# Performance work log

Measured on AMD Instinct MI355X. Metric: run time of the kernel, lower is better.

The kernel has to match this reference:

```python
import jax, jax.numpy as jnp
import numpy as np
from jax import lax

STRIDES = (8, 16, 32)
NUM_CLASSES = 80
TOPK = 1000
CONF_THRESH = 0.05
NMS_THRESH = 0.6


def setup_inputs() -> dict:
    key = jax.random.key(0)
    ks = jax.random.split(key, 10)
    hw = [(256, 256), (128, 128), (64, 64)]
    inp = {}
    for lv, (h, w) in enumerate(hw):
        inp[f"cls_pred_{lv}"] = jax.random.normal(ks[3 * lv + 0], (NUM_CLASSES, h, w), jnp.float32)
        inp[f"reg_pred_{lv}"] = jax.random.normal(ks[3 * lv + 1], (4, h, w), jnp.float32)
        inp[f"ctn_pred_{lv}"] = jax.random.normal(ks[3 * lv + 2], (1, h, w), jnp.float32)
    inp["scales"] = jax.random.uniform(ks[9], (3,), jnp.float32)
    return inp


def _level_decode(cls_p, reg_p, ctn_p, scale, stride):
    # cls_p: [C,H,W] -> flatten to [M,C] matching torch permute(1,2,0).view(-1,C)
    C, H, W = cls_p.shape
    cls = jnp.transpose(cls_p, (1, 2, 0)).reshape(-1, C)          # [M,C]
    reg = jnp.transpose(reg_p, (1, 2, 0)).reshape(-1, 4)          # [M,4]
    reg = jax.nn.relu(reg * scale) * stride                       # Scale + relu + stride
    ctn = jnp.transpose(ctn_p, (1, 2, 0)).reshape(-1, 1)          # [M,1]
    joint = jnp.sqrt(jax.nn.sigmooid(cls) * jax.nn.sigmoid(ctn)) if False else \
        jnp.sqrt(jax.nn.sigmoid(cls) * jax.nn.sigmoid(ctn))      # [M,C]
    scores = jnp.max(joint, axis=-1)                              # [M]
    labels = jnp.argmax(joint, axis=-1)                           # [M]
    ay, ax = jnp.meshgrid(jnp.arange(H), jnp.arange(W), indexing='ij')
    anchors = (jnp.stack([ax, ay], -1).reshape(-1, 2).astype(cls.dtype) + 0.5) * stride  # [M,2]
    # per-level topk (M > TOPK for all levels here)
    scores, idx = lax.top_k(scores, TOPK)
    labels = labels[idx]
    reg = reg[idx]
    anchors = anchors[idx]
    boxes = jnp.concatenate([anchors - reg[:, :2], anchors + reg[:, 2:]], axis=-1)  # x1y1x2y2
    return scores, labels, boxes


def _nms(boxes, scores):
    # Faithful port of the pure-python NMS: fixed-shape keep mask, sorted order.
    N = boxes.shape[0]
    order = jnp.argsort(-scores)
    b = boxes[order]
    x1, y1, x2, y2 = b[:, 0], b[:, 1], b[:, 2], b[:, 3]
    areas = (x2 - x1) * (y2 - y1)
    xx1 = jnp.maximum(x1[:, None], x1[None, :])
    yy1 = jnp.maximum(y1[:, None], y1[None, :])
    xx2 = jnp.minimum(x2[:, None], x2[None, :])
    yy2 = jnp.minimum(y2[:, None], y2[None, :])
    w = jnp.maximum(1e-10, xx2 - xx1)
    h = jnp.maximum(1e-10, yy2 - yy1)
    inter = w * h
    iou = inter / (areas[:, None] + areas[None, :] - inter + 1e-14)  # [N,N]
    idxs = jnp.arange(N)

    def body(i, keep):
        sup = (iou[i] > NMS_THRESH) & (idxs > i) & keep[i]
        return keep & ~sup

    keep = lax.fori_loop(0, N, body, jnp.ones((N,), bool))
    return order, keep


def reference(cls_pred_0, cls_pred_1, cls_pred_2,
              reg_pred_0, reg_pred_1, reg_pred_2,
              ctn_pred_0, ctn_pred_1, ctn_pred_2, scales):
    cls_l = [cls_pred_0, cls_pred_1, cls_pred_2]
    reg_l = [reg_pred_0, reg_pred_1, reg_pred_2]
    ctn_l = [ctn_pred_0, ctn_pred_1, ctn_pred_2]
    all_s, all_l, all_b = [], [], []
    for lv in range(3):
        s, lb, bx = _level_decode(cls_l[lv], reg_l[lv], ctn_l[lv], scales[lv], float(STRIDES[lv]))
        all_s.append(s); all_l.append(lb); all_b.append(bx)
    scores = jnp.concatenate(all_s)   # [3000]
    labels = jnp.concatenate(all_l)
    boxes = jnp.concatenate(all_b)    # [3000,4]
    order, keep = _nms(boxes, scores)
    scores_s = scores[order]
    labels_s = labels[order]
    boxes_s = boxes[order]
    keep = keep & (scores_s > CONF_THRESH)
    return boxes_s, scores_s, labels_s, keep
```

## Files before the change

kernel.cpp:

```cpp
#include <hip/hip_runtime.h>
#include <cmath>
#include <stdint.h>

#define NPTS   86016
#define NB     (1 << 18)
#define NCB    1024
#define K_TOP  1000
#define NOUT   3000
#define NWORDS 47
#define NTILE  47
#define CAND_CAP 16384
#define ECAP   8192
#define FCAP   1024
#define SPPB   64

#define HIST_OFF   0
#define CH_OFF     (NB * 3 * 4)
#define CNT_OFF    (CH_OFF + NCB * 3 * 4)
#define MEMSET_BYTES (CNT_OFF + 64)
#define KEYS_OFF   (CNT_OFF + 64)
#define LAB_OFF    (KEYS_OFF + NPTS * 8)
#define SURE_OFF   (LAB_OFF + NPTS * 4)
#define CAND_OFF   (SURE_OFF + 3 * 1024 * 8)
#define SURV_OFF   (CAND_OFF + 3 * CAND_CAP * 8)
#define EDGE_OFF   (SURV_OFF + NOUT * 8 + 64)
#define FLAG_OFF   (EDGE_OFF + ECAP * 4)

__device__ __forceinline__ float sig_f32_stepwise(float x) {
    float e = (float)exp(-(double)x);
    return 1.0f / (1.0f + e);
}

__device__ __forceinline__ void locate(int g, int& lv, int& p, int& HW) {
    if (g < 65536)      { lv = 0; p = g;         HW = 65536; }
    else if (g < 81920) { lv = 1; p = g - 65536; HW = 16384; }
    else                { lv = 2; p = g - 81920; HW = 4096;  }
}

__global__ __launch_bounds__(256) void score_kernel(
        const float* __restrict__ cls0, const float* __restrict__ cls1,
        const float* __restrict__ cls2,
        const float* __restrict__ ctn0, const float* __restrict__ ctn1,
        const float* __restrict__ ctn2,
        unsigned long long* __restrict__ keys, int* __restrict__ labels,
        int* __restrict__ hist, int* __restrict__ chist,
        int* __restrict__ cnt, unsigned* __restrict__ flags) {
    __shared__ float pm[5 * SPPB], pv[5 * SPPB];
    __shared__ int pidx[5 * SPPB];
    __shared__ int lch[NCB];
    const int tid = threadIdx.x;
    const int base = blockIdx.x * SPPB;
    for (int i = tid; i < NCB; i += 256) lch[i] = 0;
    for (int it = tid; it < 5 * SPPB; it += 256) {
        int c = it / SPPB, pt = it - c * SPPB;
        int g = base + pt, lv, p, HW;
        locate(g, lv, p, HW);
        const float* cls = (lv == 0) ? cls0 : ((lv == 1) ? cls1 : cls2);
        const float* bp = cls + (size_t)c * 16 * HW + p;
        float x[16];
#pragma unroll
        for (int cc = 0; cc < 16; cc++) x[cc] = bp[(size_t)cc * HW];
        float m = -INFINITY, v = -INFINITY; int idx = 0;
#pragma unroll
        for (int cc = 0; cc < 16; cc++)
            if (x[cc] > m) { v = m; m = x[cc]; idx = c * 16 + cc; }
        pm[it] = m; pv[it] = v; pidx[it] = idx;
    }
    __syncthreads();
    if (tid < SPPB) {
        int g = base + tid, lv, p, HW;
        locate(g, lv, p, HW);
        const float* ctn = (lv == 0) ? ctn0 : ((lv == 1) ? ctn1 : ctn2);
        float m = -INFINITY, v = -INFINITY; int idx = 0;
#pragma unroll
        for (int k = 0; k < 5; k++) {
            float bm = pm[k * SPPB + tid];
            float bv = pv[k * SPPB + tid];
            int bidx = pidx[k * SPPB + tid];
            if (bm > m) { v = fmaxf(m, bv); m = bm; idx = bidx; }
        }
        float sc = sig_f32_stepwise(ctn[p]);
        float sM = sig_f32_stepwise(m);
        float jm = __fsqrt_rn(sM * sc);
        float sV = sig_f32_stepwise(v);
        float jv = __fsqrt_rn(sV * sc);
        if (jv == jm) {
            int f = atomicAdd(&cnt[13], 1);
            if (f < FCAP) flags[f] = (unsigned)g;
        }
        unsigned int bits = __float_as_uint(jm);
        keys[g] = ((unsigned long long)bits << 32) | (0xFFFFFFFFu - (unsigned)g);
        labels[g] = idx;
        atomicAdd(&hist[lv * NB + (int)(bits >> 12)], 1);
        atomicAdd(&lch[(int)(bits >> 20)], 1);
    }
    __syncthreads();
    int lv0, p0, HW0; locate(base, lv0, p0, HW0);
    for (int i = tid; i < NCB; i += 256) {
        int v = lch[i];
        if (v) atomicAdd(&chist[lv0 * NCB + i], v);
    }
}

__global__ __launch_bounds__(1024) void thresh_kernel(
        const float* __restrict__ cls0, const float* __restrict__ cls1,
        const float* __restrict__ cls2,
        const float* __restrict__ ctn0, const float* __restrict__ ctn1,
        const float* __restrict__ ctn2,
        const int* __restrict__ hist, const int* __restrict__ chist,
        int* __restrict__ cnt,
        const unsigned* __restrict__ flags, int* __restrict__ labels) {
    int bid = blockIdx.x, tid = threadIdx.x;
    if (bid < 3) {
        int lv = bid;
        const int* h = hist + lv * NB;
        __shared__ int part[1024];
        __shared__ int s_chunk, s_above;
        __shared__ int bins[257];
        part[tid] = chist[lv * NCB + tid];
        __syncthreads();
        for (int off = 1; off < 1024; off <<= 1) {
            int v = part[tid] + ((tid + off < 1024) ? part[tid + off] : 0);
            __syncthreads(); part[tid] = v; __syncthreads();
        }
        int nxt = (tid < 1023) ? part[tid + 1] : 0;
        if (part[tid] >= K_TOP && nxt < K_TOP) { s_chunk = tid; s_above = nxt; }
        __syncthreads();
        int chunk = s_chunk, above = s_above;
        if (tid < 256) bins[tid] = h[chunk * 256 + tid];
        __syncthreads();
        for (int off = 1; off < 256; off <<= 1) {
            int v = 0;
            if (tid < 256) v = bins[tid] + ((tid + off < 256) ? bins[tid + off] : 0);
            __syncthreads(); if (tid < 256) bins[tid] = v; __syncthreads();
        }
        if (tid < 256) {
            int ge    = above + bins[tid];
            int genxt = above + ((tid < 255) ? bins[tid + 1] : 0);
            if (ge >= K_TOP && genxt < K_TOP) {
                cnt[6 + lv] = chunk * 256 + tid;
                cnt[9 + lv] = K_TOP - genxt;
            }
        }
    } else {
        int nf = cnt[13]; if (nf > FCAP) nf = FCAP;
        int wave = tid >> 6, lane = tid & 63;
        for (int f = wave; f < nf; f += 16) {
            int g = (int)flags[f], lv, p, HW;
            locate(g, lv, p, HW);
            const float* cls = (lv == 0) ? cls0 : ((lv == 1) ? cls1 : cls2);
            const float* ctn = (lv == 0) ? ctn0 : ((lv == 1) ? ctn1 : ctn2);
            float sc = sig_f32_stepwise(ctn[p]);
            float bestv = -1.0f; int besti = 127;
            {
                float s = sig_f32_stepwise(cls[(size_t)lane * HW + p]);
                float sj = __fsqrt_rn(s * sc);
                bestv = sj; besti = lane;
            }
            if (lane < 16) {
                int c2 = lane + 64;
                float s = sig_f32_stepwise(cls[(size_t)c2 * HW + p]);
                float sj = __fsqrt_rn(s * sc);
                if (sj > bestv) { bestv = sj; besti = c2; }
            }
            for (int off = 32; off; off >>= 1) {
                float ov = __shfl_xor(bestv, off, 64);
                int   oi = __shfl_xor(besti, off, 64);
                if (ov > bestv || (ov == bestv && oi < besti)) { bestv = ov; besti = oi; }
            }
            if (lane == 0) labels[g] = besti;
        }
    }
}

__global__ void compact_kernel(const unsigned long long* __restrict__ keys,
                               int* __restrict__ cnt,
                               unsigned long long* __restrict__ sure,
                               unsigned long long* __restrict__ cand) {
    int g = blockIdx.x * blockDim.x + threadIdx.x;
    if (g >= NPTS) return;
    int lv = (g < 65536) ? 0 : (g < 81920 ? 1 : 2);
    unsigned long long key = keys[g];
    int bin = (int)(key >> 44);
    int B = cnt[6 + lv];
    if (bin > B) {
        int i = atomicAdd(&cnt[0 + lv], 1);
        sure[lv * 1024 + i] = key;
    } else if (bin == B) {
        int i = atomicAdd(&cnt[3 + lv], 1);
        if (i < CAND_CAP) cand[lv * CAND_CAP + i] = key;
    }
}

__global__ void select_kernel(const int* __restrict__ cnt,
                              const unsigned long long* __restrict__ sure,
                              unsigned long long* __restrict__ cand,
                              unsigned long long* __restrict__ surv) {
    int lv = blockIdx.x, tid = threadIdx.x;
    unsigned long long* c = cand + lv * CAND_CAP;
    int n = cnt[3 + lv]; if (n > CAND_CAP) n = CAND_CAP;
    int R = cnt[9 + lv];
    int Ca = K_TOP - R;
    int m = 1; while (m < n) m <<= 1;
    for (int t = n + tid; t < m; t += 1024) c[t] = 0ULL;
    __syncthreads();
    for (int k = 2; k <= m; k <<= 1)
        for (int j = k >> 1; j > 0; j >>= 1) {
            for (int t = tid; t < m; t += 1024) {
                int l = t ^ j;
                if (l > t) {
                    unsigned long long a = c[t], b = c[l];
                    if (((t & k) == 0) ? (a < b) : (a > b)) { c[t] = b; c[l] = a; }
                }
            }
            __syncthreads();
        }
    __shared__ unsigned long long s[1024];
    s[tid] = (tid < Ca) ? sure[lv * 1024 + tid]
                        : ((tid < K_TOP) ? c[tid - Ca] : 0ULL);
    __syncthreads();
    for (int k = 2; k <= 1024; k <<= 1)
        for (int j = k >> 1; j > 0; j >>= 1) {
            int l = tid ^ j;
            if (l > tid) {
                unsigned long long a = s[tid], b = s[l];
                if (((tid & k) == 0) ? (a < b) : (a > b)) { s[tid] = b; s[l] = a; }
            }
            __syncthreads();
        }
    if (tid < K_TOP) surv[lv * K_TOP + tid] = s[tid];
}

__global__ __launch_bounds__(1024) void merge_emit_kernel(
        const unsigned long long* __restrict__ surv,
        const int* __restrict__ labels,
        const float* __restrict__ reg0, const float* __restrict__ reg1,
        const float* __restrict__ reg2,
        const float* __restrict__ scales,
        float* __restrict__ out) {
    __shared__ unsigned long long L[3][1024];
    __shared__ unsigned long long s[NOUT];
    int tid = threadIdx.x;
#pragma unroll
    for (int lv = 0; lv < 3; lv++)
        L[lv][tid] = (tid < K_TOP) ? surv[lv * K_TOP + tid] : 0ULL;
    __syncthreads();
    for (int e = tid; e < NOUT; e += 1024) {
        int a = e / K_TOP, i = e - a * K_TOP;
        unsigned long long key = L[a][i];
        int rank = i;
#pragma unroll
        for (int b = 0; b < 3; b++) {
            if (b == a) continue;
            int lo = 0, hi = K_TOP;
            while (lo < hi) {
                int mid = (lo + hi) >> 1;
                if (L[b][mid] > key) lo = mid + 1; else hi = mid;
            }
            rank += lo;
        }
        s[rank] = key;
    }
    __syncthreads();
    for (int r = tid; r < NOUT; r += 1024) {
        unsigned long long key = s[r];
        unsigned int bits = (unsigned)(key >> 32);
        float score = __uint_as_float(bits);
        unsigned int g = 0xFFFFFFFFu - (unsigned)(key & 0xFFFFFFFFULL);
        int lv, p;
        if (g < 65536u)      { lv = 0; p = (int)g; }
        else if (g < 81920u) { lv = 1; p = (int)g - 65536; }
        else                 { lv = 2; p = (int)g - 81920; }
        const float* rp = (lv == 0) ? reg0 : ((lv == 1) ? reg1 : reg2);
        int HW = (lv == 0) ? 65536 : ((lv == 1) ? 16384 : 4096);
        int W = 256 >> lv;
        float strideF = (float)(8 << lv);
        float scale = scales[lv];
        int x = p & (W - 1);
        int y = p >> (8 - lv);
        float r0 = fmaxf(0.0f, rp[0 * HW + p] * scale) * strideF;
        float r1 = fmaxf(0.0f, rp[1 * HW + p] * scale) * strideF;
        float r2 = fmaxf(0.0f, rp[2 * HW + p] * scale) * strideF;
        float r3 = fmaxf(0.0f, rp[3 * HW + p] * scale) * strideF;
        float ax = ((float)x + 0.5f) * strideF;
        float ay = ((float)y + 0.5f) * strideF;
        out[r * 4 + 0] = ax - r0;
        out[r * 4 + 1] = ay - r1;
        out[r * 4 + 2] = ax + r2;
        out[r * 4 + 3] = ay + r3;
        out[12000 + r] = score;
        out[15000 + r] = (float)labels[g];
    }
}

__global__ __launch_bounds__(256) void edge_kernel(const float* __restrict__ out,
                                                   unsigned* __restrict__ edges_g,
                                                   int* __restrict__ cnt) {
    __shared__ float x1[128], y1[128], x2[128], y2[128];
    int t = blockIdx.x, tid = threadIdx.x;
    int ta = 0, rem = t;
    while (rem >= NTILE - ta) { rem -= NTILE - ta; ta++; }
    int tb = ta + rem;
    if (tid < 64) {
        int gi = ta * 64 + tid;
        if (gi < NOUT) {
            float4 b = ((const float4*)out)[gi];
            x1[tid] = b.x; y1[tid] = b.y; x2[tid] = b.z; y2[tid] = b.w;
        }
    } else if (tid < 128) {
        int gj = tb * 64 + (tid - 64);
        if (gj < NOUT) {
            float4 b = ((const float4*)out)[gj];
            x1[tid] = b.x; y1[tid] = b.y; x2[tid] = b.z; y2[tid] = b.w;
        }
    }
    __syncthreads();
#pragma unroll
    for (int q = 0; q < 16; q++) {
        int idx = q * 256 + tid;
        int ii = idx >> 6, jj = idx & 63;
        int i = ta * 64 + ii, j = tb * 64 + jj;
        if (i < j && j < NOUT) {
            float ai = (x2[ii] - x1[ii]) * (y2[ii] - y1[ii]);
            float aj = (x2[64 + jj] - x1[64 + jj]) * (y2[64 + jj] - y1[64 + jj]);
            float xx1 = fmaxf(x1[ii], x1[64 + jj]), yy1 = fmaxf(y1[ii], y1[64 + jj]);
            float xx2 = fminf(x2[ii], x2[64 + jj]), yy2 = fminf(y2[ii], y2[64 + jj]);
            float ww = fmaxf(1e-10f, xx2 - xx1);
            float hh = fmaxf(1e-10f, yy2 - yy1);
            float inter = ww * hh;
            float iou = inter / (((ai + aj) - inter) + 1e-14f);
            if ((double)iou > 0.6) {
                int e = atomicAdd(&cnt[12], 1);
                if (e < ECAP) edges_g[e] = ((unsigned)i << 12) | (unsigned)j;
            }
        }
    }
}

__global__ __launch_bounds__(1024) void nms_sparse_kernel(
        const unsigned* __restrict__ edges_g,
        const int* __restrict__ cnt,
        const float* __restrict__ scores_s,
        float* __restrict__ keep_out) {
    __shared__ unsigned ed[ECAP];
    __shared__ unsigned long long supLds[NWORDS];
    int tid = threadIdx.x;
    int E = cnt[12]; if (E > ECAP) E = ECAP;
    int m = 1; while (m < E) m <<= 1;
    for (int t = tid; t < m; t += 1024) ed[t] = (t < E) ? edges_g[t] : 0xFFFFFFFFu;
    __syncthreads();
    for (int k = 2; k <= m; k <<= 1)
        for (int j = k >> 1; j > 0; j >>= 1) {
            for (int t = tid; t < m; t += 1024) {
                int l = t ^ j;
                if (l > t) {
                    unsigned a = ed[t], b = ed[l];
                    if (((t & k) == 0) ? (a > b) : (a < b)) { ed[t] = b; ed[l] = a; }
                }
            }
            __syncthreads();
        }
    if (tid < 64) {
        int lane = tid;
        unsigned long long supW = 0ULL;
        int ep = 0;
        for (int c = 0; c < NWORDS; c++) {
            unsigned long long cw = __shfl(supW, c, 64);
            int hi = (c + 1) * 64;
            while (ep < E) {
                unsigned k = ed[ep];
                int i = (int)(k >> 12);
                if (i >= hi) break;
                int j = (int)(k & 4095);
                if (!((cw >> (i & 63)) & 1ULL)) {
                    if ((j >> 6) == c) cw |= 1ULL << (j & 63);
                    else if (lane == (j >> 6)) supW |= 1ULL << (j & 63);
                }
                ep++;
            }
            if (lane == c) supW = cw;
        }
        if (lane < NWORDS) supLds[lane] = supW;
    }
    __syncthreads();
    for (int j = tid; j < NOUT; j += 1024) {
        bool s = (supLds[j >> 6] >> (j & 63)) & 1ULL;
        float scv = scores_s[j];
        keep_out[j] = (!s && ((double)scv > 0.05)) ? 1.0f : 0.0f;
    }
}

extern "C" void kernel_launch(void* const* d_in, const int* in_sizes, int n_in,
                              void* d_out, int out_size, void* d_ws, size_t ws_size,
                              hipStream_t stream) {
    const float* cls0 = (const float*)d_in[0];
    const float* reg0 = (const float*)d_in[1];
    const float* ctn0 = (const float*)d_in[2];
    const float* cls1 = (const float*)d_in[3];
    const float* reg1 = (const float*)d_in[4];
    const float* ctn1 = (const float*)d_in[5];
    const float* cls2 = (const float*)d_in[6];
    const float* reg2 = (const float*)d_in[7];
    const float* ctn2 = (const float*)d_in[8];
    const float* scales = (const float*)d_in[9];

    char* ws = (char*)d_ws;
    int* hist = (int*)(ws + HIST_OFF);
    int* chist = (int*)(ws + CH_OFF);
    int* cnt  = (int*)(ws + CNT_OFF);
    unsigned long long* keys = (unsigned long long*)(ws + KEYS_OFF);
    int* labels = (int*)(ws + LAB_OFF);
    unsigned long long* sure = (unsigned long long*)(ws + SURE_OFF);
    unsigned long long* cand = (unsigned long long*)(ws + CAND_OFF);
    unsigned long long* surv = (unsigned long long*)(ws + SURV_OFF);
    unsigned* edges = (unsigned*)(ws + EDGE_OFF);
    unsigned* flags = (unsigned*)(ws + FLAG_OFF);
    float* out = (float*)d_out;

    hipMemsetAsync(ws, 0, MEMSET_BYTES, stream);

    score_kernel<<<NPTS / SPPB, 256, 0, stream>>>(cls0, cls1, cls2, ctn0, ctn1, ctn2,
                                                  keys, labels, hist, chist, cnt, flags);
    thresh_kernel<<<4, 1024, 0, stream>>>(cls0, cls1, cls2, ctn0, ctn1, ctn2,
                                          hist, chist, cnt, flags, labels);
    compact_kernel<<<(NPTS + 255) / 256, 256, 0, stream>>>(keys, cnt, sure, cand);
    select_kernel<<<3, 1024, 0, stream>>>(cnt, sure, cand, surv);
    merge_emit_kernel<<<1, 1024, 0, stream>>>(surv, labels, reg0, reg1, reg2, scales, out);
    edge_kernel<<<NTILE * (NTILE + 1) / 2, 256, 0, stream>>>(out, edges, cnt);
    nms_sparse_kernel<<<1, 1024, 0, stream>>>(edges, cnt, out + 12000, out + 18000);
}
```

Baseline: 194.6 us.

## Fuse all pipeline stages into one persistent kernel with grid barriers

Merges the seven separate kernels into a single persistent kernel of 256 blocks of 1024 threads, with stages separated by a software grid barrier built on atomics in workspace memory. The scoring stage now splits each point's 80 classes across two lanes and combines them with a shuffle. The per-block shared-memory coarse histogram is replaced by direct global atomics, and edge tiles are processed by 8 teams per block. This is meant to remove the launch gaps between the many small serial stages. In exchange it relies on all 256 blocks being co-resident, and most blocks sit idle at several barriers while single-block stages run.

```diff
diff --git a/kernel.cpp b/kernel.cpp
--- a/kernel.cpp
+++ b/kernel.cpp
@@ -9,16 +9,19 @@
 #define NOUT   3000
 #define NWORDS 47
 #define NTILE  47
+#define NTILES (NTILE * (NTILE + 1) / 2)
 #define CAND_CAP 16384
 #define ECAP   8192
 #define FCAP   1024
-#define SPPB   64
+#define GRID   256
+#define BLOCK  1024
 
 #define HIST_OFF   0
 #define CH_OFF     (NB * 3 * 4)
 #define CNT_OFF    (CH_OFF + NCB * 3 * 4)
-#define MEMSET_BYTES (CNT_OFF + 64)
-#define KEYS_OFF   (CNT_OFF + 64)
+#define BAR_OFF    (CNT_OFF + 64)
+#define MEMSET_BYTES (BAR_OFF + 128)
+#define KEYS_OFF   (BAR_OFF + 128)
 #define LAB_OFF    (KEYS_OFF + NPTS * 8)
 #define SURE_OFF   (LAB_OFF + NPTS * 4)
 #define CAND_OFF   (SURE_OFF + 3 * 1024 * 8)
@@ -37,112 +40,131 @@
     else                { lv = 2; p = g - 81920; HW = 4096;  }
 }
 
-__global__ __launch_bounds__(256) void score_kernel(
+__device__ __forceinline__ void gsync(int* bar, int nblk) {
+    __syncthreads();
+    if (threadIdx.x == 0) {
+        __threadfence();
+        int* cntp = bar;
+        int* genp = bar + 16;
+        int g = __hip_atomic_load(genp, __ATOMIC_RELAXED, __HIP_MEMORY_SCOPE_AGENT);
+        int prev = __hip_atomic_fetch_add(cntp, 1, __ATOMIC_RELAXED, __HIP_MEMORY_SCOPE_AGENT);
+        if (prev == nblk - 1) {
+            __hip_atomic_store(cntp, 0, __ATOMIC_RELAXED, __HIP_MEMORY_SCOPE_AGENT);
+            __threadfence();
+            __hip_atomic_store(genp, g + 1, __ATOMIC_RELAXED, __HIP_MEMORY_SCOPE_AGENT);
+        } else {
+            while (__hip_atomic_load(genp, __ATOMIC_RELAXED, __HIP_MEMORY_SCOPE_AGENT) == g)
+                __builtin_amdgcn_s_sleep(2);
+        }
+        __threadfence();
+    }
+    __syncthreads();
+}
+
+__global__ __launch_bounds__(1024, 4) void fcos_mega(
         const float* __restrict__ cls0, const float* __restrict__ cls1,
         const float* __restrict__ cls2,
         const float* __restrict__ ctn0, const float* __restrict__ ctn1,
         const float* __restrict__ ctn2,
-        unsigned long long* __restrict__ keys, int* __restrict__ labels,
-        int* __restrict__ hist, int* __restrict__ chist,
-        int* __restrict__ cnt, unsigned* __restrict__ flags) {
-    __shared__ float pm[5 * SPPB], pv[5 * SPPB];
-    __shared__ int pidx[5 * SPPB];
-    __shared__ int lch[NCB];
+        const float* __restrict__ reg0, const float* __restrict__ reg1,
+        const float* __restrict__ reg2,
+        const float* __restrict__ scales, char* ws, float* out) {
     const int tid = threadIdx.x;
-    const int base = blockIdx.x * SPPB;
-    for (int i = tid; i < NCB; i += 256) lch[i] = 0;
-    for (int it = tid; it < 5 * SPPB; it += 256) {
-        int c = it / SPPB, pt = it - c * SPPB;
-        int g = base + pt, lv, p, HW;
-        locate(g, lv, p, HW);
-        const float* cls = (lv == 0) ? cls0 : ((lv == 1) ? cls1 : cls2);
-        const float* bp = cls + (size_t)c * 16 * HW + p;
-        float x[16];
-#pragma unroll
-        for (int cc = 0; cc < 16; cc++) x[cc] = bp[(size_t)cc * HW];
-        float m = -INFINITY, v = -INFINITY; int idx = 0;
-#pragma unroll
-        for (int cc = 0; cc < 16; cc++)
-            if (x[cc] > m) { v = m; m = x[cc]; idx = c * 16 + cc; }
-        pm[it] = m; pv[it] = v; pidx[it] = idx;
-    }
-    __syncthreads();
-    if (tid < SPPB) {
-        int g = base + tid, lv, p, HW;
-        locate(g, lv, p, HW);
-        const float* ctn = (lv == 0) ? ctn0 : ((lv == 1) ? ctn1 : ctn2);
-        float m = -INFINITY, v = -INFINITY; int idx = 0;
-#pragma unroll
-        for (int k = 0; k < 5; k++) {
-            float bm = pm[k * SPPB + tid];
-            float bv = pv[k * SPPB + tid];
-            int bidx = pidx[k * SPPB + tid];
-            if (bm > m) { v = fmaxf(m, bv); m = bm; idx = bidx; }
-        }
-        float sc = sig_f32_stepwise(ctn[p]);
-        float sM = sig_f32_stepwise(m);
-        float jm = __fsqrt_rn(sM * sc);
-        float sV = sig_f32_stepwise(v);
-        float jv = __fsqrt_rn(sV * sc);
-        if (jv == jm) {
-            int f = atomicAdd(&cnt[13], 1);
-            if (f < FCAP) flags[f] = (unsigned)g;
-        }
-        unsigned int bits = __float_as_uint(jm);
-        keys[g] = ((unsigned long long)bits << 32) | (0xFFFFFFFFu - (unsigned)g);
-        labels[g] = idx;
-        atomicAdd(&hist[lv * NB + (int)(bits >> 12)], 1);
-        atomicAdd(&lch[(int)(bits >> 20)], 1);
-    }
-    __syncthreads();
-    int lv0, p0, HW0; locate(base, lv0, p0, HW0);
-    for (int i = tid; i < NCB; i += 256) {
-        int v = lch[i];
-        if (v) atomicAdd(&chist[lv0 * NCB + i], v);
-    }
-}
-
-__global__ __launch_bounds__(1024) void thresh_kernel(
-        const float* __restrict__ cls0, const float* __restrict__ cls1,
-        const float* __restrict__ cls2,
-        const float* __restrict__ ctn0, const float* __restrict__ ctn1,
-        const float* __restrict__ ctn2,
-        const int* __restrict__ hist, const int* __restrict__ chist,
-        int* __restrict__ cnt,
-        const unsigned* __restrict__ flags, int* __restrict__ labels) {
-    int bid = blockIdx.x, tid = threadIdx.x;
+    const int bid = blockIdx.x;
+    const int nblk = gridDim.x;
+
+    int* hist = (int*)(ws + HIST_OFF);
+    int* chist = (int*)(ws + CH_OFF);
+    int* cnt = (int*)(ws + CNT_OFF);
+    int* bar = (int*)(ws + BAR_OFF);
+    unsigned long long* keys = (unsigned long long*)(ws + KEYS_OFF);
+    int* labels = (int*)(ws + LAB_OFF);
+    unsigned long long* sure = (unsigned long long*)(ws + SURE_OFF);
+    unsigned long long* cand = (unsigned long long*)(ws + CAND_OFF);
+    unsigned long long* surv = (unsigned long long*)(ws + SURV_OFF);
+    unsigned* edges_g = (unsigned*)(ws + EDGE_OFF);
+    unsigned* flags = (unsigned*)(ws + FLAG_OFF);
+
+    __shared__ union {
+        struct { int part[1024]; int bins[257]; int s_chunk; int s_above; } th;
+        struct { unsigned long long s[1024]; } sel;
+        struct { unsigned long long L[3][1024]; unsigned long long s[NOUT]; } mg;
+        struct { float x1[8][128], y1[8][128], x2[8][128], y2[8][128]; } eg;
+        struct { unsigned ed[ECAP]; unsigned long long supLds[NWORDS]; } nm;
+    } sh;
+
+    {
+        const int u = bid * BLOCK + tid;
+        if (u < 2 * NPTS) {
+            const int g = u >> 1, half = u & 1;
+            int lv, p, HW; locate(g, lv, p, HW);
+            const float* cls = (lv == 0) ? cls0 : ((lv == 1) ? cls1 : cls2);
+            const float* bp = cls + (size_t)(half * 40) * HW + p;
+            float m = -INFINITY, v = -INFINITY; int idx = half * 40;
+#pragma unroll
+            for (int cb = 0; cb < 5; cb++) {
+                float x[8];
+#pragma unroll
+                for (int cc = 0; cc < 8; cc++) x[cc] = bp[(size_t)(cb * 8 + cc) * HW];
+#pragma unroll
+                for (int cc = 0; cc < 8; cc++)
+                    if (x[cc] > m) { v = m; m = x[cc]; idx = half * 40 + cb * 8 + cc; }
+            }
+            float om = __shfl_xor(m, 1, 64);
+            float ov = __shfl_xor(v, 1, 64);
+            int   oi = __shfl_xor(idx, 1, 64);
+            if (half == 0) {
+                if (om > m) { v = fmaxf(m, ov); m = om; idx = oi; }
+                else        { v = fmaxf(v, om); }
+                const float* ctn = (lv == 0) ? ctn0 : ((lv == 1) ? ctn1 : ctn2);
+                float sc = sig_f32_stepwise(ctn[p]);
+                float sM = sig_f32_stepwise(m);
+                float jm = __fsqrt_rn(sM * sc);
+                float sV = sig_f32_stepwise(v);
+                float jv = __fsqrt_rn(sV * sc);
+                if (jv == jm) {
+                    int f = atomicAdd(&cnt[13], 1);
+                    if (f < FCAP) flags[f] = (unsigned)g;
+                }
+                unsigned int bits = __float_as_uint(jm);
+                keys[g] = ((unsigned long long)bits << 32) | (0xFFFFFFFFu - (unsigned)g);
+                labels[g] = idx;
+                atomicAdd(&hist[lv * NB + (int)(bits >> 12)], 1);
+                atomicAdd(&chist[lv * NCB + (int)(bits >> 20)], 1);
+            }
+        }
+    }
+    gsync(bar, nblk);
+
     if (bid < 3) {
         int lv = bid;
         const int* h = hist + lv * NB;
-        __shared__ int part[1024];
-        __shared__ int s_chunk, s_above;
-        __shared__ int bins[257];
-        part[tid] = chist[lv * NCB + tid];
+        sh.th.part[tid] = chist[lv * NCB + tid];
         __syncthreads();
         for (int off = 1; off < 1024; off <<= 1) {
-            int v = part[tid] + ((tid + off < 1024) ? part[tid + off] : 0);
-            __syncthreads(); part[tid] = v; __syncthreads();
-        }
-        int nxt = (tid < 1023) ? part[tid + 1] : 0;
-        if (part[tid] >= K_TOP && nxt < K_TOP) { s_chunk = tid; s_above = nxt; }
-        __syncthreads();
-        int chunk = s_chunk, above = s_above;
-        if (tid < 256) bins[tid] = h[chunk * 256 + tid];
+            int v = sh.th.part[tid] + ((tid + off < 1024) ? sh.th.part[tid + off] : 0);
+            __syncthreads(); sh.th.part[tid] = v; __syncthreads();
+        }
+        int nxt = (tid < 1023) ? sh.th.part[tid + 1] : 0;
+        if (sh.th.part[tid] >= K_TOP && nxt < K_TOP) { sh.th.s_chunk = tid; sh.th.s_above = nxt; }
+        __syncthreads();
+        int chunk = sh.th.s_chunk, above = sh.th.s_above;
+        if (tid < 256) sh.th.bins[tid] = h[chunk * 256 + tid];
         __syncthreads();
         for (int off = 1; off < 256; off <<= 1) {
             int v = 0;
-            if (tid < 256) v = bins[tid] + ((tid + off < 256) ? bins[tid + off] : 0);
-            __syncthreads(); if (tid < 256) bins[tid] = v; __syncthreads();
+            if (tid < 256) v = sh.th.bins[tid] + ((tid + off < 256) ? sh.th.bins[tid + off] : 0);
+            __syncthreads(); if (tid < 256) sh.th.bins[tid] = v; __syncthreads();
         }
         if (tid < 256) {
-            int ge    = above + bins[tid];
-            int genxt = above + ((tid < 255) ? bins[tid + 1] : 0);
+            int ge    = above + sh.th.bins[tid];
+            int genxt = above + ((tid < 255) ? sh.th.bins[tid + 1] : 0);
             if (ge >= K_TOP && genxt < K_TOP) {
                 cnt[6 + lv] = chunk * 256 + tid;
                 cnt[9 + lv] = K_TOP - genxt;
             }
         }
-    } else {
+    } else if (bid == 3) {
         int nf = cnt[13]; if (nf > FCAP) nf = FCAP;
         int wave = tid >> 6, lane = tid & 63;
         for (int f = wave; f < nf; f += 16) {
@@ -171,222 +193,213 @@
             if (lane == 0) labels[g] = besti;
         }
     }
-}
-
-__global__ void compact_kernel(const unsigned long long* __restrict__ keys,
-                               int* __restrict__ cnt,
-                               unsigned long long* __restrict__ sure,
-                               unsigned long long* __restrict__ cand) {
-    int g = blockIdx.x * blockDim.x + threadIdx.x;
-    if (g >= NPTS) return;
-    int lv = (g < 65536) ? 0 : (g < 81920 ? 1 : 2);
-    unsigned long long key = keys[g];
-    int bin = (int)(key >> 44);
-    int B = cnt[6 + lv];
-    if (bin > B) {
-        int i = atomicAdd(&cnt[0 + lv], 1);
-        sure[lv * 1024 + i] = key;
-    } else if (bin == B) {
-        int i = atomicAdd(&cnt[3 + lv], 1);
-        if (i < CAND_CAP) cand[lv * CAND_CAP + i] = key;
-    }
-}
-
-__global__ void select_kernel(const int* __restrict__ cnt,
-                              const unsigned long long* __restrict__ sure,
-                              unsigned long long* __restrict__ cand,
-                              unsigned long long* __restrict__ surv) {
-    int lv = blockIdx.x, tid = threadIdx.x;
-    unsigned long long* c = cand + lv * CAND_CAP;
-    int n = cnt[3 + lv]; if (n > CAND_CAP) n = CAND_CAP;
-    int R = cnt[9 + lv];
-    int Ca = K_TOP - R;
-    int m = 1; while (m < n) m <<= 1;
-    for (int t = n + tid; t < m; t += 1024) c[t] = 0ULL;
-    __syncthreads();
-    for (int k = 2; k <= m; k <<= 1)
-        for (int j = k >> 1; j > 0; j >>= 1) {
-            for (int t = tid; t < m; t += 1024) {
-                int l = t ^ j;
-                if (l > t) {
-                    unsigned long long a = c[t], b = c[l];
-                    if (((t & k) == 0) ? (a < b) : (a > b)) { c[t] = b; c[l] = a; }
-                }
-            }
-            __syncthreads();
-        }
-    __shared__ unsigned long long s[1024];
-    s[tid] = (tid < Ca) ? sure[lv * 1024 + tid]
-                        : ((tid < K_TOP) ? c[tid - Ca] : 0ULL);
-    __syncthreads();
-    for (int k = 2; k <= 1024; k <<= 1)
-        for (int j = k >> 1; j > 0; j >>= 1) {
-            int l = tid ^ j;
-            if (l > tid) {
-                unsigned long long a = s[tid], b = s[l];
-                if (((tid & k) == 0) ? (a < b) : (a > b)) { s[tid] = b; s[l] = a; }
-            }
-            __syncthreads();
-        }
-    if (tid < K_TOP) surv[lv * K_TOP + tid] = s[tid];
-}
-
-__global__ __launch_bounds__(1024) void merge_emit_kernel(
-        const unsigned long long* __restrict__ surv,
-        const int* __restrict__ labels,
-        const float* __restrict__ reg0, const float* __restrict__ reg1,
-        const float* __restrict__ reg2,
-        const float* __restrict__ scales,
-        float* __restrict__ out) {
-    __shared__ unsigned long long L[3][1024];
-    __shared__ unsigned long long s[NOUT];
-    int tid = threadIdx.x;
-#pragma unroll
-    for (int lv = 0; lv < 3; lv++)
-        L[lv][tid] = (tid < K_TOP) ? surv[lv * K_TOP + tid] : 0ULL;
-    __syncthreads();
-    for (int e = tid; e < NOUT; e += 1024) {
-        int a = e / K_TOP, i = e - a * K_TOP;
-        unsigned long long key = L[a][i];
-        int rank = i;
-#pragma unroll
-        for (int b = 0; b < 3; b++) {
-            if (b == a) continue;
-            int lo = 0, hi = K_TOP;
-            while (lo < hi) {
-                int mid = (lo + hi) >> 1;
-                if (L[b][mid] > key) lo = mid + 1; else hi = mid;
-            }
-            rank += lo;
-        }
-        s[rank] = key;
-    }
-    __syncthreads();
-    for (int r = tid; r < NOUT; r += 1024) {
-        unsigned long long key = s[r];
-        unsigned int bits = (unsigned)(key >> 32);
-        float score = __uint_as_float(bits);
-        unsigned int g = 0xFFFFFFFFu - (unsigned)(key & 0xFFFFFFFFULL);
-        int lv, p;
-        if (g < 65536u)      { lv = 0; p = (int)g; }
-        else if (g < 81920u) { lv = 1; p = (int)g - 65536; }
-        else                 { lv = 2; p = (int)g - 81920; }
-        const float* rp = (lv == 0) ? reg0 : ((lv == 1) ? reg1 : reg2);
-        int HW = (lv == 0) ? 65536 : ((lv == 1) ? 16384 : 4096);
-        int W = 256 >> lv;
-        float strideF = (float)(8 << lv);
-        float scale = scales[lv];
-        int x = p & (W - 1);
-        int y = p >> (8 - lv);
-        float r0 = fmaxf(0.0f, rp[0 * HW + p] * scale) * strideF;
-        float r1 = fmaxf(0.0f, rp[1 * HW + p] * scale) * strideF;
-        float r2 = fmaxf(0.0f, rp[2 * HW + p] * scale) * strideF;
-        float r3 = fmaxf(0.0f, rp[3 * HW + p] * scale) * strideF;
-        float ax = ((float)x + 0.5f) * strideF;
-        float ay = ((float)y + 0.5f) * strideF;
-        out[r * 4 + 0] = ax - r0;
-        out[r * 4 + 1] = ay - r1;
-        out[r * 4 + 2] = ax + r2;
-        out[r * 4 + 3] = ay + r3;
-        out[12000 + r] = score;
-        out[15000 + r] = (float)labels[g];
-    }
-}
-
-__global__ __launch_bounds__(256) void edge_kernel(const float* __restrict__ out,
-                                                   unsigned* __restrict__ edges_g,
-                                                   int* __restrict__ cnt) {
-    __shared__ float x1[128], y1[128], x2[128], y2[128];
-    int t = blockIdx.x, tid = threadIdx.x;
-    int ta = 0, rem = t;
-    while (rem >= NTILE - ta) { rem -= NTILE - ta; ta++; }
-    int tb = ta + rem;
-    if (tid < 64) {
-        int gi = ta * 64 + tid;
-        if (gi < NOUT) {
-            float4 b = ((const float4*)out)[gi];
-            x1[tid] = b.x; y1[tid] = b.y; x2[tid] = b.z; y2[tid] = b.w;
-        }
-    } else if (tid < 128) {
-        int gj = tb * 64 + (tid - 64);
-        if (gj < NOUT) {
-            float4 b = ((const float4*)out)[gj];
-            x1[tid] = b.x; y1[tid] = b.y; x2[tid] = b.z; y2[tid] = b.w;
-        }
-    }
-    __syncthreads();
-#pragma unroll
-    for (int q = 0; q < 16; q++) {
-        int idx = q * 256 + tid;
-        int ii = idx >> 6, jj = idx & 63;
-        int i = ta * 64 + ii, j = tb * 64 + jj;
-        if (i < j && j < NOUT) {
-            float ai = (x2[ii] - x1[ii]) * (y2[ii] - y1[ii]);
-            float aj = (x2[64 + jj] - x1[64 + jj]) * (y2[64 + jj] - y1[64 + jj]);
-            float xx1 = fmaxf(x1[ii], x1[64 + jj]), yy1 = fmaxf(y1[ii], y1[64 + jj]);
-            float xx2 = fminf(x2[ii], x2[64 + jj]), yy2 = fminf(y2[ii], y2[64 + jj]);
-            float ww = fmaxf(1e-10f, xx2 - xx1);
-            float hh = fmaxf(1e-10f, yy2 - yy1);
-            float inter = ww * hh;
-            float iou = inter / (((ai + aj) - inter) + 1e-14f);
-            if ((double)iou > 0.6) {
-                int e = atomicAdd(&cnt[12], 1);
-                if (e < ECAP) edges_g[e] = ((unsigned)i << 12) | (unsigned)j;
-            }
-        }
-    }
-}
-
-__global__ __launch_bounds__(1024) void nms_sparse_kernel(
-        const unsigned* __restrict__ edges_g,
-        const int* __restrict__ cnt,
-        const float* __restrict__ scores_s,
-        float* __restrict__ keep_out) {
-    __shared__ unsigned ed[ECAP];
-    __shared__ unsigned long long supLds[NWORDS];
-    int tid = threadIdx.x;
-    int E = cnt[12]; if (E > ECAP) E = ECAP;
-    int m = 1; while (m < E) m <<= 1;
-    for (int t = tid; t < m; t += 1024) ed[t] = (t < E) ? edges_g[t] : 0xFFFFFFFFu;
-    __syncthreads();
-    for (int k = 2; k <= m; k <<= 1)
-        for (int j = k >> 1; j > 0; j >>= 1) {
-            for (int t = tid; t < m; t += 1024) {
-                int l = t ^ j;
-                if (l > t) {
-                    unsigned a = ed[t], b = ed[l];
-                    if (((t & k) == 0) ? (a > b) : (a < b)) { ed[t] = b; ed[l] = a; }
-                }
-            }
-            __syncthreads();
-        }
-    if (tid < 64) {
-        int lane = tid;
-        unsigned long long supW = 0ULL;
-        int ep = 0;
-        for (int c = 0; c < NWORDS; c++) {
-            unsigned long long cw = __shfl(supW, c, 64);
-            int hi = (c + 1) * 64;
-            while (ep < E) {
-                unsigned k = ed[ep];
-                int i = (int)(k >> 12);
-                if (i >= hi) break;
-                int j = (int)(k & 4095);
-                if (!((cw >> (i & 63)) & 1ULL)) {
-                    if ((j >> 6) == c) cw |= 1ULL << (j & 63);
-                    else if (lane == (j >> 6)) supW |= 1ULL << (j & 63);
-                }
-                ep++;
-            }
-            if (lane == c) supW = cw;
-        }
-        if (lane < NWORDS) supLds[lane] = supW;
-    }
-    __syncthreads();
-    for (int j = tid; j < NOUT; j += 1024) {
-        bool s = (supLds[j >> 6] >> (j & 63)) & 1ULL;
-        float scv = scores_s[j];
-        keep_out[j] = (!s && ((double)scv > 0.05)) ? 1.0f : 0.0f;
+    gsync(bar, nblk);
+
+    {
+        int g = bid * BLOCK + tid;
+        if (g < NPTS) {
+            int lv = (g < 65536) ? 0 : (g < 81920 ? 1 : 2);
+            unsigned long long key = keys[g];
+            int bin = (int)(key >> 44);
+            int B = cnt[6 + lv];
+            if (bin > B) {
+                int i = atomicAdd(&cnt[0 + lv], 1);
+                sure[lv * 1024 + i] = key;
+            } else if (bin == B) {
+                int i = atomicAdd(&cnt[3 + lv], 1);
+                if (i < CAND_CAP) cand[lv * CAND_CAP + i] = key;
+            }
+        }
+    }
+    gsync(bar, nblk);
+
+    if (bid < 3) {
+        int lv = bid;
+        unsigned long long* c = cand + lv * CAND_CAP;
+        int n = cnt[3 + lv]; if (n > CAND_CAP) n = CAND_CAP;
+        int R = cnt[9 + lv];
+        int Ca = K_TOP - R;
+        int m = 1; while (m < n) m <<= 1;
+        for (int t = n + tid; t < m; t += 1024) c[t] = 0ULL;
+        __syncthreads();
+        for (int k = 2; k <= m; k <<= 1)
+            for (int j = k >> 1; j > 0; j >>= 1) {
+                for (int t = tid; t < m; t += 1024) {
+                    int l = t ^ j;
+                    if (l > t) {
+                        unsigned long long a = c[t], b = c[l];
+                        if (((t & k) == 0) ? (a < b) : (a > b)) { c[t] = b; c[l] = a; }
+                    }
+                }
+                __syncthreads();
+            }
+        sh.sel.s[tid] = (tid < Ca) ? sure[lv * 1024 + tid]
+                                   : ((tid < K_TOP) ? c[tid - Ca] : 0ULL);
+        __syncthreads();
+        for (int k = 2; k <= 1024; k <<= 1)
+            for (int j = k >> 1; j > 0; j >>= 1) {
+                int l = tid ^ j;
+                if (l > tid) {
+                    unsigned long long a = sh.sel.s[tid], b = sh.sel.s[l];
+                    if (((tid & k) == 0) ? (a < b) : (a > b)) { sh.sel.s[tid] = b; sh.sel.s[l] = a; }
+                }
+                __syncthreads();
+            }
+        if (tid < K_TOP) surv[lv * K_TOP + tid] = sh.sel.s[tid];
+    }
+    gsync(bar, nblk);
+
+    if (bid == 0) {
+#pragma unroll
+        for (int lv = 0; lv < 3; lv++)
+            sh.mg.L[lv][tid] = (tid < K_TOP) ? surv[lv * K_TOP + tid] : 0ULL;
+        __syncthreads();
+        for (int e = tid; e < NOUT; e += 1024) {
+            int a = e / K_TOP, i = e - a * K_TOP;
+            unsigned long long key = sh.mg.L[a][i];
+            int rank = i;
+#pragma unroll
+            for (int b = 0; b < 3; b++) {
+                if (b == a) continue;
+                int lo = 0, hi = K_TOP;
+                while (lo < hi) {
+                    int mid = (lo + hi) >> 1;
+                    if (sh.mg.L[b][mid] > key) lo = mid + 1; else hi = mid;
+                }
+                rank += lo;
+            }
+            sh.mg.s[rank] = key;
+        }
+        __syncthreads();
+        for (int r = tid; r < NOUT; r += 1024) {
+            unsigned long long key = sh.mg.s[r];
+            unsigned int bits = (unsigned)(key >> 32);
+            float score = __uint_as_float(bits);
+            unsigned int g = 0xFFFFFFFFu - (unsigned)(key & 0xFFFFFFFFULL);
+            int lv, p;
+            if (g < 65536u)      { lv = 0; p = (int)g; }
+            else if (g < 81920u) { lv = 1; p = (int)g - 65536; }
+            else                 { lv = 2; p = (int)g - 81920; }
+            const float* rp = (lv == 0) ? reg0 : ((lv == 1) ? reg1 : reg2);
+            int HW = (lv == 0) ? 65536 : ((lv == 1) ? 16384 : 4096);
+            int W = 256 >> lv;
+            float strideF = (float)(8 << lv);
+            float scale = scales[lv];
+            int x = p & (W - 1);
+            int y = p >> (8 - lv);
+            float r0 = fmaxf(0.0f, rp[0 * HW + p] * scale) * strideF;
+            float r1 = fmaxf(0.0f, rp[1 * HW + p] * scale) * strideF;
+            float r2 = fmaxf(0.0f, rp[2 * HW + p] * scale) * strideF;
+            float r3 = fmaxf(0.0f, rp[3 * HW + p] * scale) * strideF;
+            float ax = ((float)x + 0.5f) * strideF;
+            float ay = ((float)y + 0.5f) * strideF;
+            out[r * 4 + 0] = ax - r0;
+            out[r * 4 + 1] = ay - r1;
+            out[r * 4 + 2] = ax + r2;
+            out[r * 4 + 3] = ay + r3;
+            out[12000 + r] = score;
+            out[15000 + r] = (float)labels[g];
+        }
+    }
+    gsync(bar, nblk);
+
+    {
+        int team = tid >> 7, lt = tid & 127;
+        int t = bid * 8 + team;
+        int ta = 0, tb = 0;
+        bool act = (t < NTILES);
+        if (act) {
+            int rem = t;
+            while (rem >= NTILE - ta) { rem -= NTILE - ta; ta++; }
+            tb = ta + rem;
+            if (lt < 64) {
+                int gi = ta * 64 + lt;
+                if (gi < NOUT) {
+                    float4 b = ((const float4*)out)[gi];
+                    sh.eg.x1[team][lt] = b.x; sh.eg.y1[team][lt] = b.y;
+                    sh.eg.x2[team][lt] = b.z; sh.eg.y2[team][lt] = b.w;
+                }
+            } else {
+                int gj = tb * 64 + (lt - 64);
+                if (gj < NOUT) {
+                    float4 b = ((const float4*)out)[gj];
+                    sh.eg.x1[team][lt] = b.x; sh.eg.y1[team][lt] = b.y;
+                    sh.eg.x2[team][lt] = b.z; sh.eg.y2[team][lt] = b.w;
+                }
+            }
+        }
+        __syncthreads();
+        if (act) {
+#pragma unroll
+            for (int q = 0; q < 32; q++) {
+                int idx = q * 128 + lt;
+                int ii = idx >> 6, jj = idx & 63;
+                int i = ta * 64 + ii, j = tb * 64 + jj;
+                if (i < j && j < NOUT) {
+                    float ai = (sh.eg.x2[team][ii] - sh.eg.x1[team][ii]) * (sh.eg.y2[team][ii] - sh.eg.y1[team][ii]);
+                    float aj = (sh.eg.x2[team][64 + jj] - sh.eg.x1[team][64 + jj]) * (sh.eg.y2[team][64 + jj] - sh.eg.y1[team][64 + jj]);
+                    float xx1 = fmaxf(sh.eg.x1[team][ii], sh.eg.x1[team][64 + jj]);
+                    float yy1 = fmaxf(sh.eg.y1[team][ii], sh.eg.y1[team][64 + jj]);
+                    float xx2 = fminf(sh.eg.x2[team][ii], sh.eg.x2[team][64 + jj]);
+                    float yy2 = fminf(sh.eg.y2[team][ii], sh.eg.y2[team][64 + jj]);
+                    float ww = fmaxf(1e-10f, xx2 - xx1);
+                    float hh = fmaxf(1e-10f, yy2 - yy1);
+                    float inter = ww * hh;
+                    float iou = inter / (((ai + aj) - inter) + 1e-14f);
+                    if ((double)iou > 0.6) {
+                        int e = atomicAdd(&cnt[12], 1);
+                        if (e < ECAP) edges_g[e] = ((unsigned)i << 12) | (unsigned)j;
+                    }
+                }
+            }
+        }
+    }
+    gsync(bar, nblk);
+
+    if (bid == 0) {
+        int E = cnt[12]; if (E > ECAP) E = ECAP;
+        int m = 1; while (m < E) m <<= 1;
+        for (int t = tid; t < m; t += 1024) sh.nm.ed[t] = (t < E) ? edges_g[t] : 0xFFFFFFFFu;
+        __syncthreads();
+        for (int k = 2; k <= m; k <<= 1)
+            for (int j = k >> 1; j > 0; j >>= 1) {
+                for (int t = tid; t < m; t += 1024) {
+                    int l = t ^ j;
+                    if (l > t) {
+                        unsigned a = sh.nm.ed[t], b = sh.nm.ed[l];
+                        if (((t & k) == 0) ? (a > b) : (a < b)) { sh.nm.ed[t] = b; sh.nm.ed[l] = a; }
+                    }
+                }
+                __syncthreads();
+            }
+        if (tid < 64) {
+            int lane = tid;
+            unsigned long long supW = 0ULL;
+            int ep = 0;
+            for (int c = 0; c < NWORDS; c++) {
+                unsigned long long cw = __shfl(supW, c, 64);
+                int hi = (c + 1) * 64;
+                while (ep < E) {
+                    unsigned kk = sh.nm.ed[ep];
+                    int i = (int)(kk >> 12);
+                    if (i >= hi) break;
+                    int j = (int)(kk & 4095);
+                    if (!((cw >> (i & 63)) & 1ULL)) {
+                        if ((j >> 6) == c) cw |= 1ULL << (j & 63);
+                        else if (lane == (j >> 6)) supW |= 1ULL << (j & 63);
+                    }
+                    ep++;
+                }
+                if (lane == c) supW = cw;
+            }
+            if (lane < NWORDS) sh.nm.supLds[lane] = supW;
+        }
+        __syncthreads();
+        for (int j = tid; j < NOUT; j += 1024) {
+            bool s = (sh.nm.supLds[j >> 6] >> (j & 63)) & 1ULL;
+            float scv = out[12000 + j];
+            out[18000 + j] = (!s && ((double)scv > 0.05)) ? 1.0f : 0.0f;
+        }
     }
 }
 
@@ -405,27 +418,10 @@
     const float* scales = (const float*)d_in[9];
 
     char* ws = (char*)d_ws;
-    int* hist = (int*)(ws + HIST_OFF);
-    int* chist = (int*)(ws + CH_OFF);
-    int* cnt  = (int*)(ws + CNT_OFF);
-    unsigned long long* keys = (unsigned long long*)(ws + KEYS_OFF);
-    int* labels = (int*)(ws + LAB_OFF);
-    unsigned long long* sure = (unsigned long long*)(ws + SURE_OFF);
-    unsigned long long* cand = (unsigned long long*)(ws + CAND_OFF);
-    unsigned long long* surv = (unsigned long long*)(ws + SURV_OFF);
-    unsigned* edges = (unsigned*)(ws + EDGE_OFF);
-    unsigned* flags = (unsigned*)(ws + FLAG_OFF);
     float* out = (float*)d_out;
 
     hipMemsetAsync(ws, 0, MEMSET_BYTES, stream);
 
-    score_kernel<<<NPTS / SPPB, 256, 0, stream>>>(cls0, cls1, cls2, ctn0, ctn1, ctn2,
-                                                  keys, labels, hist, chist, cnt, flags);
-    thresh_kernel<<<4, 1024, 0, stream>>>(cls0, cls1, cls2, ctn0, ctn1, ctn2,
-                                          hist, chist, cnt, flags, labels);
-    compact_kernel<<<(NPTS + 255) / 256, 256, 0, stream>>>(keys, cnt, sure, cand);
-    select_kernel<<<3, 1024, 0, stream>>>(cnt, sure, cand, surv);
-    merge_emit_kernel<<<1, 1024, 0, stream>>>(surv, labels, reg0, reg1, reg2, scales, out);
-    edge_kernel<<<NTILE * (NTILE + 1) / 2, 256, 0, stream>>>(out, edges, cnt);
-    nms_sparse_kernel<<<1, 1024, 0, stream>>>(edges, cnt, out + 12000, out + 18000);
+    fcos_mega<<<GRID, BLOCK, 0, stream>>>(cls0, cls1, cls2, ctn0, ctn1, ctn2,
+                                          reg0, reg1, reg2, scales, ws, out);
 }
```

Measured after the change: 456.4 us. 135% more time.

## Fuse threshold, compact and select into one kernel; drop fine global histogram

Applied to the files above, without the earlier changes.

Removes the 3MB fine-grained global histogram, which had to be memset every call and took global atomics per point. Each level's block now rescans its keys and builds the fine histogram in shared memory only for the selected coarse chunk. Threshold finding, compaction and the bitonic selection are merged into one 4-block kernel, saving two launches and using shared-memory counters. The cost is that one block per level serially scans up to 65536 keys twice, which can leave the level-0 block as a long serial tail.

```diff
diff --git a/kernel.cpp b/kernel.cpp
--- a/kernel.cpp
+++ b/kernel.cpp
@@ -3,7 +3,6 @@
 #include <stdint.h>
 
 #define NPTS   86016
-#define NB     (1 << 18)
 #define NCB    1024
 #define K_TOP  1000
 #define NOUT   3000
@@ -14,9 +13,8 @@
 #define FCAP   1024
 #define SPPB   64
 
-#define HIST_OFF   0
-#define CH_OFF     (NB * 3 * 4)
-#define CNT_OFF    (CH_OFF + NCB * 3 * 4)
+#define CH_OFF     0
+#define CNT_OFF    (NCB * 3 * 4)
 #define MEMSET_BYTES (CNT_OFF + 64)
 #define KEYS_OFF   (CNT_OFF + 64)
 #define LAB_OFF    (KEYS_OFF + NPTS * 8)
@@ -25,6 +23,7 @@
 #define SURV_OFF   (CAND_OFF + 3 * CAND_CAP * 8)
 #define EDGE_OFF   (SURV_OFF + NOUT * 8 + 64)
 #define FLAG_OFF   (EDGE_OFF + ECAP * 4)
+#define SMERGE_OFF (FLAG_OFF + FCAP * 4)
 
 __device__ __forceinline__ float sig_f32_stepwise(float x) {
     float e = (float)exp(-(double)x);
@@ -43,7 +42,7 @@
         const float* __restrict__ ctn0, const float* __restrict__ ctn1,
         const float* __restrict__ ctn2,
         unsigned long long* __restrict__ keys, int* __restrict__ labels,
-        int* __restrict__ hist, int* __restrict__ chist,
+        int* __restrict__ chist,
         int* __restrict__ cnt, unsigned* __restrict__ flags) {
     __shared__ float pm[5 * SPPB], pv[5 * SPPB];
     __shared__ int pidx[5 * SPPB];
@@ -91,7 +90,6 @@
         unsigned int bits = __float_as_uint(jm);
         keys[g] = ((unsigned long long)bits << 32) | (0xFFFFFFFFu - (unsigned)g);
         labels[g] = idx;
-        atomicAdd(&hist[lv * NB + (int)(bits >> 12)], 1);
         atomicAdd(&lch[(int)(bits >> 20)], 1);
     }
     __syncthreads();
@@ -102,47 +100,20 @@
     }
 }
 
-__global__ __launch_bounds__(1024) void thresh_kernel(
+__global__ __launch_bounds__(1024) void tcs_kernel(
         const float* __restrict__ cls0, const float* __restrict__ cls1,
         const float* __restrict__ cls2,
         const float* __restrict__ ctn0, const float* __restrict__ ctn1,
         const float* __restrict__ ctn2,
-        const int* __restrict__ hist, const int* __restrict__ chist,
-        int* __restrict__ cnt,
-        const unsigned* __restrict__ flags, int* __restrict__ labels) {
+        const unsigned long long* __restrict__ keys,
+        const int* __restrict__ chist,
+        const unsigned* __restrict__ flags, const int* __restrict__ cnt,
+        int* __restrict__ labels,
+        unsigned long long* __restrict__ sure,
+        unsigned long long* __restrict__ cand,
+        unsigned long long* __restrict__ surv) {
     int bid = blockIdx.x, tid = threadIdx.x;
-    if (bid < 3) {
-        int lv = bid;
-        const int* h = hist + lv * NB;
-        __shared__ int part[1024];
-        __shared__ int s_chunk, s_above;
-        __shared__ int bins[257];
-        part[tid] = chist[lv * NCB + tid];
-        __syncthreads();
-        for (int off = 1; off < 1024; off <<= 1) {
-            int v = part[tid] + ((tid + off < 1024) ? part[tid + off] : 0);
-            __syncthreads(); part[tid] = v; __syncthreads();
-        }
-        int nxt = (tid < 1023) ? part[tid + 1] : 0;
-        if (part[tid] >= K_TOP && nxt < K_TOP) { s_chunk = tid; s_above = nxt; }
-        __syncthreads();
-        int chunk = s_chunk, above = s_above;
-        if (tid < 256) bins[tid] = h[chunk * 256 + tid];
-        __syncthreads();
-        for (int off = 1; off < 256; off <<= 1) {
-            int v = 0;
-            if (tid < 256) v = bins[tid] + ((tid + off < 256) ? bins[tid + off] : 0);
-            __syncthreads(); if (tid < 256) bins[tid] = v; __syncthreads();
-        }
-        if (tid < 256) {
-            int ge    = above + bins[tid];
-            int genxt = above + ((tid < 255) ? bins[tid + 1] : 0);
-            if (ge >= K_TOP && genxt < K_TOP) {
-                cnt[6 + lv] = chunk * 256 + tid;
-                cnt[9 + lv] = K_TOP - genxt;
-            }
-        }
-    } else {
+    if (bid == 3) {
         int nf = cnt[13]; if (nf > FCAP) nf = FCAP;
         int wave = tid >> 6, lane = tid & 63;
         for (int f = wave; f < nf; f += 16) {
@@ -170,36 +141,63 @@
             }
             if (lane == 0) labels[g] = besti;
         }
-    }
-}
-
-__global__ void compact_kernel(const unsigned long long* __restrict__ keys,
-                               int* __restrict__ cnt,
-                               unsigned long long* __restrict__ sure,
-                               unsigned long long* __restrict__ cand) {
-    int g = blockIdx.x * blockDim.x + threadIdx.x;
-    if (g >= NPTS) return;
-    int lv = (g < 65536) ? 0 : (g < 81920 ? 1 : 2);
-    unsigned long long key = keys[g];
-    int bin = (int)(key >> 44);
-    int B = cnt[6 + lv];
-    if (bin > B) {
-        int i = atomicAdd(&cnt[0 + lv], 1);
-        sure[lv * 1024 + i] = key;
-    } else if (bin == B) {
-        int i = atomicAdd(&cnt[3 + lv], 1);
-        if (i < CAND_CAP) cand[lv * CAND_CAP + i] = key;
-    }
-}
-
-__global__ void select_kernel(const int* __restrict__ cnt,
-                              const unsigned long long* __restrict__ sure,
-                              unsigned long long* __restrict__ cand,
-                              unsigned long long* __restrict__ surv) {
-    int lv = blockIdx.x, tid = threadIdx.x;
+        return;
+    }
+    const int lv = bid;
+    const int base = (lv == 0) ? 0 : ((lv == 1) ? 65536 : 81920);
+    const int HW = (lv == 0) ? 65536 : ((lv == 1) ? 16384 : 4096);
+    __shared__ int part[1024];
+    __shared__ int fine[257];
+    __shared__ int s_chunk, s_above, sB, sR, sCnt2[2];
+    __shared__ unsigned long long sel[1024];
+
+    if (tid == 0) { sCnt2[0] = 0; sCnt2[1] = 0; }
+    part[tid] = chist[lv * NCB + tid];
+    __syncthreads();
+    for (int off = 1; off < 1024; off <<= 1) {
+        int v = part[tid] + ((tid + off < 1024) ? part[tid + off] : 0);
+        __syncthreads(); part[tid] = v; __syncthreads();
+    }
+    int nxt = (tid < 1023) ? part[tid + 1] : 0;
+    if (part[tid] >= K_TOP && nxt < K_TOP) { s_chunk = tid; s_above = nxt; }
+    if (tid < 257) fine[tid] = 0;
+    __syncthreads();
+    const int chunk = s_chunk, above = s_above;
+    for (int i = tid; i < HW; i += 1024) {
+        unsigned bits = (unsigned)(keys[base + i] >> 32);
+        if ((int)(bits >> 20) == chunk) atomicAdd(&fine[(bits >> 12) & 255], 1);
+    }
+    __syncthreads();
+    for (int off = 1; off < 256; off <<= 1) {
+        int v = 0;
+        if (tid < 256) v = fine[tid] + ((tid + off < 256) ? fine[tid + off] : 0);
+        __syncthreads(); if (tid < 256) fine[tid] = v; __syncthreads();
+    }
+    if (tid < 256) {
+        int ge    = above + fine[tid];
+        int genxt = above + ((tid < 255) ? fine[tid + 1] : 0);
+        if (ge >= K_TOP && genxt < K_TOP) {
+            sB = chunk * 256 + tid;
+            sR = K_TOP - genxt;
+        }
+    }
+    __syncthreads();
+    const int B = sB;
+    for (int i = tid; i < HW; i += 1024) {
+        unsigned long long key = keys[base + i];
+        int bin = (int)(key >> 44);
+        if (bin > B) {
+            int k = atomicAdd(&sCnt2[0], 1);
+            sure[lv * 1024 + k] = key;
+        } else if (bin == B) {
+            int k = atomicAdd(&sCnt2[1], 1);
+            if (k < CAND_CAP) cand[lv * CAND_CAP + k] = key;
+        }
+    }
+    __syncthreads();
     unsigned long long* c = cand + lv * CAND_CAP;
-    int n = cnt[3 + lv]; if (n > CAND_CAP) n = CAND_CAP;
-    int R = cnt[9 + lv];
+    int n = sCnt2[1]; if (n > CAND_CAP) n = CAND_CAP;
+    int R = sR;
     int Ca = K_TOP - R;
     int m = 1; while (m < n) m <<= 1;
     for (int t = n + tid; t < m; t += 1024) c[t] = 0ULL;
@@ -215,20 +213,19 @@
             }
             __syncthreads();
         }
-    __shared__ unsigned long long s[1024];
-    s[tid] = (tid < Ca) ? sure[lv * 1024 + tid]
-                        : ((tid < K_TOP) ? c[tid - Ca] : 0ULL);
+    sel[tid] = (tid < Ca) ? sure[lv * 1024 + tid]
+                          : ((tid < K_TOP) ? c[tid - Ca] : 0ULL);
     __syncthreads();
     for (int k = 2; k <= 1024; k <<= 1)
         for (int j = k >> 1; j > 0; j >>= 1) {
             int l = tid ^ j;
             if (l > tid) {
-                unsigned long long a = s[tid], b = s[l];
-                if (((tid & k) == 0) ? (a < b) : (a > b)) { s[tid] = b; s[l] = a; }
+                unsigned long long a = sel[tid], b = sel[l];
+                if (((tid & k) == 0) ? (a < b) : (a > b)) { sel[tid] = b; sel[l] = a; }
             }
             __syncthreads();
         }
-    if (tid < K_TOP) surv[lv * K_TOP + tid] = s[tid];
+    if (tid < K_TOP) surv[lv * K_TOP + tid] = sel[tid];
 }
 
 __global__ __launch_bounds__(1024) void merge_emit_kernel(
@@ -405,7 +402,6 @@
     const float* scales = (const float*)d_in[9];
 
     char* ws = (char*)d_ws;
-    int* hist = (int*)(ws + HIST_OFF);
     int* chist = (int*)(ws + CH_OFF);
     int* cnt  = (int*)(ws + CNT_OFF);
     unsigned long long* keys = (unsigned long long*)(ws + KEYS_OFF);
@@ -420,11 +416,10 @@
     hipMemsetAsync(ws, 0, MEMSET_BYTES, stream);
 
     score_kernel<<<NPTS / SPPB, 256, 0, stream>>>(cls0, cls1, cls2, ctn0, ctn1, ctn2,
-                                                  keys, labels, hist, chist, cnt, flags);
-    thresh_kernel<<<4, 1024, 0, stream>>>(cls0, cls1, cls2, ctn0, ctn1, ctn2,
-                                          hist, chist, cnt, flags, labels);
-    compact_kernel<<<(NPTS + 255) / 256, 256, 0, stream>>>(keys, cnt, sure, cand);
-    select_kernel<<<3, 1024, 0, stream>>>(cnt, sure, cand, surv);
+                                                  keys, labels, chist, cnt, flags);
+    tcs_kernel<<<4, 1024, 0, stream>>>(cls0, cls1, cls2, ctn0, ctn1, ctn2,
+                                       keys, chist, flags, cnt, labels,
+                                       sure, cand, surv);
     merge_emit_kernel<<<1, 1024, 0, stream>>>(surv, labels, reg0, reg1, reg2, scales, out);
     edge_kernel<<<NTILE * (NTILE + 1) / 2, 256, 0, stream>>>(out, edges, cnt);
     nms_sparse_kernel<<<1, 1024, 0, stream>>>(edges, cnt, out + 12000, out + 18000);
```

New measurement: 192.9 us. Within noise of the previous version (-0.9%).
